# Performance work log

Measured on AMD Instinct MI355X. Metric: run time of the kernel, lower is better.

The kernel has to match this reference:

```python
import jax, jax.numpy as jnp
import numpy as np

B, C, R = 1024, 256, 7          # batch, channels, ROI feature map res
PATCH, DIL = 16, 2              # correlation patch size, dilation_patch
REP = 1024                      # representation_size
FLAT = PATCH * PATCH * R * R    # 12544 = fc1 input dim


def setup_inputs() -> dict:
    key = jax.random.key(0)
    k = jax.random.split(key, 8)
    return {
        "patch1": jax.random.normal(k[0], (B, C, R, R), dtype=jnp.float32),
        "patch2": jax.random.normal(k[1], (B, C, R, R), dtype=jnp.float32),
        "W1": jax.random.normal(k[2], (REP, FLAT), dtype=jnp.float32) * 0.01,
        "b1": jnp.zeros((REP,), dtype=jnp.float32),
        "W2": jax.random.normal(k[3], (REP, REP), dtype=jnp.float32) * 0.02,
        "b2": jnp.zeros((REP,), dtype=jnp.float32),
        "W3": jax.random.normal(k[4], (4, REP), dtype=jnp.float32) * 0.02,
        "b3": jnp.zeros((4,), dtype=jnp.float32),
    }


def _correlate(p1, p2):
    """SpatialCorrelationSampler(patch_size=16, dilation_patch=2), kernel=1, stride=1.
    out[b, pi, pj, i, j] = sum_c p1[b,c,i,j] * p2[b,c, i+(pi-8)*2, j+(pj-8)*2]
    (zero outside bounds). Returns [B, PATCH*PATCH, R, R]."""
    pad = (PATCH // 2) * DIL  # 16; displacements span [-16, 14]
    p2p = jnp.pad(p2, ((0, 0), (0, 0), (pad, pad), (pad, pad)))  # [B,C,39,39]
    outs = []
    for pi in range(PATCH):
        for pj in range(PATCH):
            # shifted window: row offset (pi-8)*2 + pad = 2*pi, same for cols
            win = p2p[:, :, DIL * pi:DIL * pi + R, DIL * pj:DIL * pj + R]
            outs.append(jnp.einsum('bchw,bchw->bhw', p1, win))
    return jnp.stack(outs, axis=1)  # [B, 256, 7, 7] -> matches torch flatten order


def reference(patch1, patch2, W1, b1, W2, b2, W3, b3):
    x = _correlate(patch1, patch2).reshape(patch1.shape[0], -1)  # [B, 12544]
    x = jax.nn.relu(x @ W1.T + b1)
    x = jax.nn.relu(x @ W2.T + b2)
    pred_boxes = x @ W3.T + b3  # [B, 4]
    return pred_boxes
```

## Files before the change

### kernel.cpp

```cpp
#include <hip/hip_runtime.h>

#define BATCH 1024
#define RR    49
#define SP    12544
#define KVALID 625
#define KPAD   640
#define REP_N  1024

typedef __attribute__((ext_vector_type(4))) float f32x4;
typedef __attribute__((ext_vector_type(8))) short s16x8;

__device__ __forceinline__ unsigned short f2bf_rne(float f) {
    unsigned int u = __float_as_uint(f);
    unsigned int r = u + 0x7FFFu + ((u >> 16) & 1u);
    return (unsigned short)(r >> 16);
}
__device__ __forceinline__ float bf2f(unsigned short h) {
    return __uint_as_float(((unsigned int)h) << 16);
}
__device__ __forceinline__ void split2(float v, unsigned short& h, unsigned short& l) {
    h = f2bf_rne(v);
    l = f2bf_rne(v - bf2f(h));
}
__device__ __forceinline__ unsigned int cvtpk_bf16(float a, float b) {
    unsigned int r;
    asm("v_cvt_pk_bf16_f32 %0, %1, %2" : "=v"(r) : "v"(a), "v"(b));
    return r;
}
__device__ __forceinline__ void cvt8(const float* v, s16x8& hv, s16x8& lv) {
    unsigned int* hp = (unsigned int*)&hv;
    unsigned int* lp = (unsigned int*)&lv;
    #pragma unroll
    for (int i = 0; i < 4; ++i) {
        float v0 = v[2 * i], v1 = v[2 * i + 1];
        unsigned int ph = cvtpk_bf16(v0, v1);
        float h0 = __uint_as_float(ph << 16);
        float h1 = __uint_as_float(ph & 0xFFFF0000u);
        unsigned int pl = cvtpk_bf16(v0 - h0, v1 - h1);
        hp[i] = ph; lp[i] = pl;
    }
}

__device__ __forceinline__ void dec25(int u, int& i, int& d) {
    int ii = (u >= 4) + (u >= 7) + (u >= 11) + (u >= 14) + (u >= 18) + (u >= 21);
    int cum = (7 * ii + 1) >> 1;
    i = ii;
    d = 2 * (u - cum) + (ii & 1);
}
__device__ __forceinline__ int enc25(int i, int d) {
    return ((7 * i + 1) >> 1) + ((d - (i & 1)) >> 1);
}

__device__ __forceinline__ int kflat_of(int a) {
    int ar = a / 25, ac = a % 25;
    int i, dy, j, dx;
    dec25(ar, i, dy);
    dec25(ac, j, dx);
    int pi = (dy + 16 - i) >> 1;
    int pj = (dx + 16 - j) >> 1;
    return (pi * 16 + pj) * 49 + i * 7 + j;
}

#define MM(d, a, b) d = __builtin_amdgcn_mfma_f32_16x16x32_bf16(a, b, d, 0, 0, 0)

__global__ __launch_bounds__(256) void corr_gram_kernel(
    const float* __restrict__ p1, const float* __restrict__ p2,
    unsigned short* __restrict__ xh, unsigned short* __restrict__ xl)
{
    __shared__ unsigned short SXh[KPAD];
    __shared__ unsigned short SXl[KPAD];

    const int b = blockIdx.x;
    const int t = threadIdx.x;
    const float* P1 = p1 + (size_t)b * SP;
    const float* P2 = p2 + (size_t)b * SP;

    const int wv   = t >> 6;
    const int lane = t & 63;
    const int wr = (wv >> 1) * 32;
    const int wc = (wv & 1) * 32;
    const int fr = lane & 15;
    const int fg = (lane >> 4) * 8;

    const int sa0 = wr + fr;
    const int sa1 = min(wr + 16 + fr, 48);
    const int sb0 = wc + fr;
    const int sb1 = min(wc + 16 + fr, 48);

    const float* pa0 = P1 + fg * 49 + sa0;
    const float* pa1 = P1 + fg * 49 + sa1;
    const float* pb0 = P2 + fg * 49 + sb0;
    const float* pb1 = P2 + fg * 49 + sb1;

    for (int i = t; i < KPAD; i += 256) { SXh[i] = 0; SXl[i] = 0; }

    f32x4 acc00 = {}, acc01 = {}, acc10 = {}, acc11 = {};

    #pragma unroll
    for (int cc = 0; cc < 4; ++cc) {
        #pragma unroll
        for (int ks = 0; ks < 2; ++ks) {
            const int co = (cc * 64 + ks * 32) * 49;
            float a0f[8], a1f[8], b0f[8], b1f[8];
            #pragma unroll
            for (int i = 0; i < 8; ++i) {
                a0f[i] = pa0[co + i * 49];
                a1f[i] = pa1[co + i * 49];
                b0f[i] = pb0[co + i * 49];
                b1f[i] = pb1[co + i * 49];
            }
            s16x8 ah0, al0, ah1, al1, bh0, bl0, bh1, bl1;
            cvt8(a0f, ah0, al0);
            cvt8(a1f, ah1, al1);
            cvt8(b0f, bh0, bl0);
            cvt8(b1f, bh1, bl1);

            MM(acc00, ah0, bh0); MM(acc00, ah0, bl0); MM(acc00, al0, bh0);
            MM(acc01, ah0, bh1); MM(acc01, ah0, bl1); MM(acc01, al0, bh1);
            MM(acc10, ah1, bh0); MM(acc10, ah1, bl0); MM(acc10, al1, bh0);
            MM(acc11, ah1, bh1); MM(acc11, ah1, bl1); MM(acc11, al1, bh1);
        }
    }

    const int arow = (lane >> 4) * 4;
    #pragma unroll
    for (int nf = 0; nf < 2; ++nf) {
        const int n = wc + nf * 16 + fr;
        #pragma unroll
        for (int mf = 0; mf < 2; ++mf) {
            const f32x4 a = (nf == 0) ? (mf == 0 ? acc00 : acc10)
                                      : (mf == 0 ? acc01 : acc11);
            #pragma unroll
            for (int r = 0; r < 4; ++r) {
                const int m = wr + mf * 16 + arow + r;
                if (m < RR && n < RR) {
                    const int i  = m / 7, jj = m - i * 7;
                    const int dy = n / 7, dx = n - dy * 7;
                    if ((((i + dy) | (jj + dx)) & 1) == 0) {
                        const int aidx = enc25(i, dy) * 25 + enc25(jj, dx);
                        unsigned short h, l;
                        split2(a[r], h, l);
                        SXh[aidx] = h; SXl[aidx] = l;
                    }
                }
            }
        }
    }
    __syncthreads();

    unsigned int* rh = (unsigned int*)(xh + (size_t)b * KPAD);
    unsigned int* rl = (unsigned int*)(xl + (size_t)b * KPAD);
    const unsigned int* sh = (const unsigned int*)SXh;
    const unsigned int* sl = (const unsigned int*)SXl;
    for (int i = t; i < KPAD / 2; i += 256) { rh[i] = sh[i]; rl[i] = sl[i]; }
}

__global__ __launch_bounds__(256) void prep_w1_kernel(
    const float* __restrict__ W1,
    unsigned short* __restrict__ wh, unsigned short* __restrict__ wl)
{
    int idx = blockIdx.x * 256 + threadIdx.x;
    int n = idx / KPAD, a = idx - n * KPAD;
    float v = 0.f;
    if (a < KVALID) v = W1[(size_t)n * SP + kflat_of(a)];
    unsigned short h, l;
    split2(v, h, l);
    wh[idx] = h; wl[idx] = l;
}

__global__ __launch_bounds__(256) void prep_w2_kernel(
    const float* __restrict__ W2,
    unsigned short* __restrict__ wh, unsigned short* __restrict__ wl)
{
    int idx = (blockIdx.x * 256 + threadIdx.x) * 4;
    float4 v = *(const float4*)&W2[idx];
    unsigned short h0, l0, h1, l1, h2, l2, h3, l3;
    split2(v.x, h0, l0); split2(v.y, h1, l1);
    split2(v.z, h2, l2); split2(v.w, h3, l3);
    ushort4 hv = make_ushort4(h0, h1, h2, h3);
    ushort4 lv = make_ushort4(l0, l1, l2, l3);
    *(ushort4*)&wh[idx] = hv;
    *(ushort4*)&wl[idx] = lv;
}

template<bool SPLIT_OUT>
__global__ __launch_bounds__(256) void gemm_mfma(
    const unsigned short* __restrict__ Xh, const unsigned short* __restrict__ Xl, int ldx,
    const unsigned short* __restrict__ Wh, const unsigned short* __restrict__ Wl, int ldw,
    const float* __restrict__ bias, int K,
    float* __restrict__ Yf, unsigned short* __restrict__ Yh, unsigned short* __restrict__ Yl,
    int ldy)
{
    __shared__ unsigned short As[2][64][72];
    __shared__ unsigned short Bs[2][64][72];

    const int t = threadIdx.x;
    const int m_base = blockIdx.y * 64;
    const int n_base = blockIdx.x * 64;

    const int trow = t >> 2;
    const int tc   = (t & 3) * 8;

    const unsigned short* xh_p = Xh + (size_t)(m_base + trow) * ldx + tc;
    const unsigned short* xl_p = Xl + (size_t)(m_base + trow) * ldx + tc;
    const unsigned short* wh_p = Wh + (size_t)(n_base + trow) * ldw + tc;
    const unsigned short* wl_p = Wl + (size_t)(n_base + trow) * ldw + tc;

    const int wv   = t >> 6;
    const int lane = t & 63;
    const int wr = (wv >> 1) * 32;
    const int wc = (wv & 1) * 32;
    const int fr = lane & 15;
    const int fg = (lane >> 4) * 8;

    f32x4 acc00 = {}, acc01 = {}, acc10 = {}, acc11 = {};

    for (int k0 = 0; k0 < K; k0 += 64) {
        s16x8 vxh0 = *(const s16x8*)(xh_p + k0);
        s16x8 vxh1 = *(const s16x8*)(xh_p + k0 + 32);
        s16x8 vxl0 = *(const s16x8*)(xl_p + k0);
        s16x8 vxl1 = *(const s16x8*)(xl_p + k0 + 32);
        s16x8 vwh0 = *(const s16x8*)(wh_p + k0);
        s16x8 vwh1 = *(const s16x8*)(wh_p + k0 + 32);
        s16x8 vwl0 = *(const s16x8*)(wl_p + k0);
        s16x8 vwl1 = *(const s16x8*)(wl_p + k0 + 32);
        __syncthreads();
        *(s16x8*)&As[0][trow][tc]      = vxh0;
        *(s16x8*)&As[0][trow][tc + 32] = vxh1;
        *(s16x8*)&As[1][trow][tc]      = vxl0;
        *(s16x8*)&As[1][trow][tc + 32] = vxl1;
        *(s16x8*)&Bs[0][trow][tc]      = vwh0;
        *(s16x8*)&Bs[0][trow][tc + 32] = vwh1;
        *(s16x8*)&Bs[1][trow][tc]      = vwl0;
        *(s16x8*)&Bs[1][trow][tc + 32] = vwl1;
        __syncthreads();

        #pragma unroll
        for (int ks = 0; ks < 2; ++ks) {
            const int ko = ks * 32 + fg;
            s16x8 ah0 = *(const s16x8*)&As[0][wr + fr][ko];
            s16x8 ah1 = *(const s16x8*)&As[0][wr + 16 + fr][ko];
            s16x8 al0 = *(const s16x8*)&As[1][wr + fr][ko];
            s16x8 al1 = *(const s16x8*)&As[1][wr + 16 + fr][ko];
            s16x8 bh0 = *(const s16x8*)&Bs[0][wc + fr][ko];
            s16x8 bh1 = *(const s16x8*)&Bs[0][wc + 16 + fr][ko];
            s16x8 bl0 = *(const s16x8*)&Bs[1][wc + fr][ko];
            s16x8 bl1 = *(const s16x8*)&Bs[1][wc + 16 + fr][ko];

            MM(acc00, ah0, bh0); MM(acc00, ah0, bl0); MM(acc00, al0, bh0);
            MM(acc01, ah0, bh1); MM(acc01, ah0, bl1); MM(acc01, al0, bh1);
            MM(acc10, ah1, bh0); MM(acc10, ah1, bl0); MM(acc10, al1, bh0);
            MM(acc11, ah1, bh1); MM(acc11, ah1, bl1); MM(acc11, al1, bh1);
        }
    }

    const int arow = (lane >> 4) * 4;
    #pragma unroll
    for (int nf = 0; nf < 2; ++nf) {
        const int col = n_base + wc + nf * 16 + fr;
        const float bv = bias[col];
        #pragma unroll
        for (int mf = 0; mf < 2; ++mf) {
            const f32x4 a = (nf == 0) ? (mf == 0 ? acc00 : acc10)
                                      : (mf == 0 ? acc01 : acc11);
            #pragma unroll
            for (int r = 0; r < 4; ++r) {
                const int row = m_base + wr + mf * 16 + arow + r;
                float v = fmaxf(a[r] + bv, 0.f);
                if (SPLIT_OUT) {
                    unsigned short h, l;
                    split2(v, h, l);
                    Yh[(size_t)row * ldy + col] = h;
                    Yl[(size_t)row * ldy + col] = l;
                } else {
                    Yf[(size_t)row * ldy + col] = v;
                }
            }
        }
    }
}

__global__ __launch_bounds__(256) void head_kernel(
    const float* __restrict__ h2, const float* __restrict__ W3,
    const float* __restrict__ b3, float* __restrict__ out)
{
    const int b = blockIdx.x;
    const int t = threadIdx.x;
    const float* row = h2 + (size_t)b * REP_N;

    float a0 = 0.f, a1 = 0.f, a2 = 0.f, a3 = 0.f;
    for (int k = t; k < REP_N; k += 256) {
        float x = row[k];
        a0 = fmaf(x, W3[k],             a0);
        a1 = fmaf(x, W3[REP_N + k],     a1);
        a2 = fmaf(x, W3[2 * REP_N + k], a2);
        a3 = fmaf(x, W3[3 * REP_N + k], a3);
    }
    #pragma unroll
    for (int off = 32; off > 0; off >>= 1) {
        a0 += __shfl_down(a0, off);
        a1 += __shfl_down(a1, off);
        a2 += __shfl_down(a2, off);
        a3 += __shfl_down(a3, off);
    }
    __shared__ float red[4][4];
    int wid = t >> 6, lane = t & 63;
    if (lane == 0) { red[wid][0] = a0; red[wid][1] = a1; red[wid][2] = a2; red[wid][3] = a3; }
    __syncthreads();
    if (t < 4) {
        out[b * 4 + t] = red[0][t] + red[1][t] + red[2][t] + red[3][t] + b3[t];
    }
}

extern "C" void kernel_launch(void* const* d_in, const int* in_sizes, int n_in,
                              void* d_out, int out_size, void* d_ws, size_t ws_size,
                              hipStream_t stream) {
    const float* p1 = (const float*)d_in[0];
    const float* p2 = (const float*)d_in[1];
    const float* W1 = (const float*)d_in[2];
    const float* b1 = (const float*)d_in[3];
    const float* W2 = (const float*)d_in[4];
    const float* b2 = (const float*)d_in[5];
    const float* W3 = (const float*)d_in[6];
    const float* b3 = (const float*)d_in[7];
    float* out = (float*)d_out;

    char* ws = (char*)d_ws;
    unsigned short* xh  = (unsigned short*)(ws + 0);
    unsigned short* xl  = (unsigned short*)(ws + 1310720);
    unsigned short* w1h = (unsigned short*)(ws + 2621440);
    unsigned short* w1l = (unsigned short*)(ws + 3932160);
    float*          h2  = (float*)(ws + 0);
    unsigned short* h1h = (unsigned short*)(ws + 5242880);
    unsigned short* h1l = (unsigned short*)(ws + 7340032);
    unsigned short* w2h = (unsigned short*)(ws + 9437184);
    unsigned short* w2l = (unsigned short*)(ws + 11534336);

    corr_gram_kernel<<<BATCH, 256, 0, stream>>>(p1, p2, xh, xl);
    prep_w1_kernel<<<(REP_N * KPAD) / 256, 256, 0, stream>>>(W1, w1h, w1l);
    prep_w2_kernel<<<(REP_N * REP_N) / (256 * 4), 256, 0, stream>>>(W2, w2h, w2l);

    gemm_mfma<true><<<dim3(16, 16), 256, 0, stream>>>(
        xh, xl, KPAD, w1h, w1l, KPAD, b1, KPAD,
        (float*)nullptr, h1h, h1l, REP_N);

    gemm_mfma<false><<<dim3(16, 16), 256, 0, stream>>>(
        h1h, h1l, REP_N, w2h, w2l, REP_N, b2, REP_N,
        h2, (unsigned short*)nullptr, (unsigned short*)nullptr, REP_N);

    head_kernel<<<BATCH, 256, 0, stream>>>(h2, W3, b3, out);
}
```

Before: 66.72 us.

## Split correlation Gram over channel halves with a separate reduction kernel

The per-batch correlation Gram kernel is split along the channel dimension into two blocks per batch. Each block writes fp32 partial sums to workspace, and a new reduce kernel sums them and does the bf16 hi/lo split. The goal is more blocks in flight and shorter per-block latency for the memory-bound correlation stage. The cost is an extra kernel launch plus an extra round trip of the partials through global memory.

Result: slower. 78.60 us (+17.8%).

```diff
diff --git a/kernel.cpp b/kernel.cpp
--- a/kernel.cpp
+++ b/kernel.cpp
@@ -6,6 +6,7 @@
 #define KVALID 625
 #define KPAD   640
 #define REP_N  1024
+#define KSPLIT 2
 
 typedef __attribute__((ext_vector_type(4))) float f32x4;
 typedef __attribute__((ext_vector_type(8))) short s16x8;
@@ -63,18 +64,18 @@
 
 #define MM(d, a, b) d = __builtin_amdgcn_mfma_f32_16x16x32_bf16(a, b, d, 0, 0, 0)
 
-__global__ __launch_bounds__(256) void corr_gram_kernel(
+__global__ __launch_bounds__(256, 8) void corr_gram_partial(
     const float* __restrict__ p1, const float* __restrict__ p2,
-    unsigned short* __restrict__ xh, unsigned short* __restrict__ xl)
-{
-    __shared__ unsigned short SXh[KPAD];
-    __shared__ unsigned short SXl[KPAD];
+    float* __restrict__ pg)
+{
+    __shared__ float SXf[KPAD];
 
     const int b = blockIdx.x;
+    const int q = blockIdx.y;
+    const float* P1 = p1 + (size_t)b * SP + q * (256 / KSPLIT) * RR;
+    const float* P2 = p2 + (size_t)b * SP + q * (256 / KSPLIT) * RR;
+
     const int t = threadIdx.x;
-    const float* P1 = p1 + (size_t)b * SP;
-    const float* P2 = p2 + (size_t)b * SP;
-
     const int wv   = t >> 6;
     const int lane = t & 63;
     const int wr = (wv >> 1) * 32;
@@ -87,39 +88,36 @@
     const int sb0 = wc + fr;
     const int sb1 = min(wc + 16 + fr, 48);
 
-    const float* pa0 = P1 + fg * 49 + sa0;
-    const float* pa1 = P1 + fg * 49 + sa1;
-    const float* pb0 = P2 + fg * 49 + sb0;
-    const float* pb1 = P2 + fg * 49 + sb1;
-
-    for (int i = t; i < KPAD; i += 256) { SXh[i] = 0; SXl[i] = 0; }
+    const float* pa0 = P1 + fg * RR + sa0;
+    const float* pa1 = P1 + fg * RR + sa1;
+    const float* pb0 = P2 + fg * RR + sb0;
+    const float* pb1 = P2 + fg * RR + sb1;
+
+    for (int i = t; i < KPAD; i += 256) SXf[i] = 0.f;
 
     f32x4 acc00 = {}, acc01 = {}, acc10 = {}, acc11 = {};
 
     #pragma unroll
-    for (int cc = 0; cc < 4; ++cc) {
+    for (int kk = 0; kk < (256 / KSPLIT) / 32; ++kk) {
+        const int co = kk * 32 * RR;
+        float a0f[8], a1f[8], b0f[8], b1f[8];
         #pragma unroll
-        for (int ks = 0; ks < 2; ++ks) {
-            const int co = (cc * 64 + ks * 32) * 49;
-            float a0f[8], a1f[8], b0f[8], b1f[8];
-            #pragma unroll
-            for (int i = 0; i < 8; ++i) {
-                a0f[i] = pa0[co + i * 49];
-                a1f[i] = pa1[co + i * 49];
-                b0f[i] = pb0[co + i * 49];
-                b1f[i] = pb1[co + i * 49];
-            }
-            s16x8 ah0, al0, ah1, al1, bh0, bl0, bh1, bl1;
-            cvt8(a0f, ah0, al0);
-            cvt8(a1f, ah1, al1);
-            cvt8(b0f, bh0, bl0);
-            cvt8(b1f, bh1, bl1);
-
-            MM(acc00, ah0, bh0); MM(acc00, ah0, bl0); MM(acc00, al0, bh0);
-            MM(acc01, ah0, bh1); MM(acc01, ah0, bl1); MM(acc01, al0, bh1);
-            MM(acc10, ah1, bh0); MM(acc10, ah1, bl0); MM(acc10, al1, bh0);
-            MM(acc11, ah1, bh1); MM(acc11, ah1, bl1); MM(acc11, al1, bh1);
+        for (int i = 0; i < 8; ++i) {
+            a0f[i] = pa0[co + i * RR];
+            a1f[i] = pa1[co + i * RR];
+            b0f[i] = pb0[co + i * RR];
+            b1f[i] = pb1[co + i * RR];
         }
+        s16x8 ah0, al0, ah1, al1, bh0, bl0, bh1, bl1;
+        cvt8(a0f, ah0, al0);
+        cvt8(a1f, ah1, al1);
+        cvt8(b0f, bh0, bl0);
+        cvt8(b1f, bh1, bl1);
+
+        MM(acc00, ah0, bh0); MM(acc00, ah0, bl0); MM(acc00, al0, bh0);
+        MM(acc01, ah0, bh1); MM(acc01, ah0, bl1); MM(acc01, al0, bh1);
+        MM(acc10, ah1, bh0); MM(acc10, ah1, bl0); MM(acc10, al1, bh0);
+        MM(acc11, ah1, bh1); MM(acc11, ah1, bl1); MM(acc11, al1, bh1);
     }
 
     const int arow = (lane >> 4) * 4;
@@ -138,9 +136,7 @@
                     const int dy = n / 7, dx = n - dy * 7;
                     if ((((i + dy) | (jj + dx)) & 1) == 0) {
                         const int aidx = enc25(i, dy) * 25 + enc25(jj, dx);
-                        unsigned short h, l;
-                        split2(a[r], h, l);
-                        SXh[aidx] = h; SXl[aidx] = l;
+                        SXf[aidx] = a[r];
                     }
                 }
             }
@@ -148,11 +144,23 @@
     }
     __syncthreads();
 
-    unsigned int* rh = (unsigned int*)(xh + (size_t)b * KPAD);
-    unsigned int* rl = (unsigned int*)(xl + (size_t)b * KPAD);
-    const unsigned int* sh = (const unsigned int*)SXh;
-    const unsigned int* sl = (const unsigned int*)SXl;
-    for (int i = t; i < KPAD / 2; i += 256) { rh[i] = sh[i]; rl[i] = sl[i]; }
+    float* dst = pg + ((size_t)b * KSPLIT + q) * KPAD;
+    for (int i = t; i < KPAD; i += 256) dst[i] = SXf[i];
+}
+
+__global__ __launch_bounds__(256) void reduce_x_kernel(
+    const float* __restrict__ pg,
+    unsigned short* __restrict__ xh, unsigned short* __restrict__ xl)
+{
+    int idx = blockIdx.x * 256 + threadIdx.x;
+    int b = idx / KPAD, a = idx - b * KPAD;
+    float s = 0.f;
+    #pragma unroll
+    for (int qq = 0; qq < KSPLIT; ++qq)
+        s += pg[((size_t)b * KSPLIT + qq) * KPAD + a];
+    unsigned short h, l;
+    split2(s, h, l);
+    xh[idx] = h; xl[idx] = l;
 }
 
 __global__ __launch_bounds__(256) void prep_w1_kernel(
@@ -335,10 +343,12 @@
     unsigned short* h1l = (unsigned short*)(ws + 7340032);
     unsigned short* w2h = (unsigned short*)(ws + 9437184);
     unsigned short* w2l = (unsigned short*)(ws + 11534336);
-
-    corr_gram_kernel<<<BATCH, 256, 0, stream>>>(p1, p2, xh, xl);
+    float*          pg  = (float*)(ws + 13631488);
+
+    corr_gram_partial<<<dim3(BATCH, KSPLIT), 256, 0, stream>>>(p1, p2, pg);
     prep_w1_kernel<<<(REP_N * KPAD) / 256, 256, 0, stream>>>(W1, w1h, w1l);
     prep_w2_kernel<<<(REP_N * REP_N) / (256 * 4), 256, 0, stream>>>(W2, w2h, w2l);
+    reduce_x_kernel<<<(BATCH * KPAD) / 256, 256, 0, stream>>>(pg, xh, xl);
 
     gemm_mfma<true><<<dim3(16, 16), 256, 0, stream>>>(
         xh, xl, KPAD, w1h, w1l, KPAD, b1, KPAD,
```

## Stage correlation inputs through padded LDS with register prefetch of next chunk

Applied to the files above, without the earlier changes.

The gram kernel used to read p1/p2 directly from global memory with strided scalar loads, one per MFMA operand element. It now loads each 64-channel chunk cooperatively with coalesced loads into registers and stores it into LDS padded to 53 floats per row to avoid bank conflicts. It prefetches the next chunk into registers while the MFMAs run on the current one. This adds about 27 KB of LDS, extra barriers and register pressure, and launch bounds now request 4 blocks per SM.

Result: slower. 70.23 us (+5.3%).

```diff
diff --git a/kernel.cpp b/kernel.cpp
--- a/kernel.cpp
+++ b/kernel.cpp
@@ -6,6 +6,7 @@
 #define KVALID 625
 #define KPAD   640
 #define REP_N  1024
+#define LP    53
 
 typedef __attribute__((ext_vector_type(4))) float f32x4;
 typedef __attribute__((ext_vector_type(8))) short s16x8;
@@ -63,10 +64,12 @@
 
 #define MM(d, a, b) d = __builtin_amdgcn_mfma_f32_16x16x32_bf16(a, b, d, 0, 0, 0)
 
-__global__ __launch_bounds__(256) void corr_gram_kernel(
+__global__ __launch_bounds__(256, 4) void corr_gram_kernel(
     const float* __restrict__ p1, const float* __restrict__ p2,
     unsigned short* __restrict__ xh, unsigned short* __restrict__ xl)
 {
+    __shared__ float T1[64 * LP];
+    __shared__ float T2[64 * LP];
     __shared__ unsigned short SXh[KPAD];
     __shared__ unsigned short SXl[KPAD];
 
@@ -86,28 +89,55 @@
     const int sa1 = min(wr + 16 + fr, 48);
     const int sb0 = wc + fr;
     const int sb1 = min(wc + 16 + fr, 48);
-
-    const float* pa0 = P1 + fg * 49 + sa0;
-    const float* pa1 = P1 + fg * 49 + sa1;
-    const float* pb0 = P2 + fg * 49 + sb0;
-    const float* pb1 = P2 + fg * 49 + sb1;
+    const int ra0 = fg * LP + sa0;
+    const int ra1 = fg * LP + sa1;
+    const int rb0 = fg * LP + sb0;
+    const int rb1 = fg * LP + sb1;
 
     for (int i = t; i < KPAD; i += 256) { SXh[i] = 0; SXl[i] = 0; }
 
+    float r1[13], r2[13];
+    #pragma unroll
+    for (int k = 0; k < 13; ++k) {
+        const int g = t + k * 256;
+        if (g < 3136) { r1[k] = P1[g]; r2[k] = P2[g]; }
+    }
+
     f32x4 acc00 = {}, acc01 = {}, acc10 = {}, acc11 = {};
 
     #pragma unroll
     for (int cc = 0; cc < 4; ++cc) {
+        __syncthreads();
+        #pragma unroll
+        for (int k = 0; k < 13; ++k) {
+            const int g = t + k * 256;
+            if (g < 3136) {
+                const int addr = g + 4 * (g / 49);
+                T1[addr] = r1[k];
+                T2[addr] = r2[k];
+            }
+        }
+        __syncthreads();
+
+        if (cc < 3) {
+            const int off = (cc + 1) * 3136;
+            #pragma unroll
+            for (int k = 0; k < 13; ++k) {
+                const int g = t + k * 256;
+                if (g < 3136) { r1[k] = P1[off + g]; r2[k] = P2[off + g]; }
+            }
+        }
+
         #pragma unroll
         for (int ks = 0; ks < 2; ++ks) {
-            const int co = (cc * 64 + ks * 32) * 49;
+            const int ko = ks * 32 * LP;
             float a0f[8], a1f[8], b0f[8], b1f[8];
             #pragma unroll
             for (int i = 0; i < 8; ++i) {
-                a0f[i] = pa0[co + i * 49];
-                a1f[i] = pa1[co + i * 49];
-                b0f[i] = pb0[co + i * 49];
-                b1f[i] = pb1[co + i * 49];
+                a0f[i] = T1[ra0 + ko + i * LP];
+                a1f[i] = T1[ra1 + ko + i * LP];
+                b0f[i] = T2[rb0 + ko + i * LP];
+                b1f[i] = T2[rb1 + ko + i * LP];
             }
             s16x8 ah0, al0, ah1, al1, bh0, bl0, bh1, bl1;
             cvt8(a0f, ah0, al0);
```

## Compute correlation Gram only within spatial parity classes via LDS staging

Applied to the files above, without the earlier changes.

The correlation kernel used to compute the full 49x49 Gram matrix per batch item with four MFMA tiles per wave and then discard entries with mismatched parity. Now each wave handles one of the four (row, column) parity classes, which needs only a single 16x16 tile, so MFMA work drops to a quarter. Inputs are loaded with coalesced float4 reads and staged through padded LDS tiles one 64-channel chunk at a time, with the next chunk prefetched into registers. The cost is extra LDS traffic and two barriers per chunk, plus a larger shared-memory footprint that may lower occupancy.

After: 66.42 us. Within noise of the previous version (-0.4%).

```diff
diff --git a/kernel.cpp b/kernel.cpp
--- a/kernel.cpp
+++ b/kernel.cpp
@@ -6,6 +6,7 @@
 #define KVALID 625
 #define KPAD   640
 #define REP_N  1024
+#define LP    53
 
 typedef __attribute__((ext_vector_type(4))) float f32x4;
 typedef __attribute__((ext_vector_type(8))) short s16x8;
@@ -63,10 +64,12 @@
 
 #define MM(d, a, b) d = __builtin_amdgcn_mfma_f32_16x16x32_bf16(a, b, d, 0, 0, 0)
 
-__global__ __launch_bounds__(256) void corr_gram_kernel(
+__global__ __launch_bounds__(256) void corr_parity_kernel(
     const float* __restrict__ p1, const float* __restrict__ p2,
     unsigned short* __restrict__ xh, unsigned short* __restrict__ xl)
 {
+    __shared__ float T1[64 * LP];
+    __shared__ float T2[64 * LP];
     __shared__ unsigned short SXh[KPAD];
     __shared__ unsigned short SXl[KPAD];
 
@@ -77,72 +80,91 @@
 
     const int wv   = t >> 6;
     const int lane = t & 63;
-    const int wr = (wv >> 1) * 32;
-    const int wc = (wv & 1) * 32;
-    const int fr = lane & 15;
-    const int fg = (lane >> 4) * 8;
-
-    const int sa0 = wr + fr;
-    const int sa1 = min(wr + 16 + fr, 48);
-    const int sb0 = wc + fr;
-    const int sb1 = min(wc + 16 + fr, 48);
-
-    const float* pa0 = P1 + fg * 49 + sa0;
-    const float* pa1 = P1 + fg * 49 + sa1;
-    const float* pb0 = P2 + fg * 49 + sb0;
-    const float* pb1 = P2 + fg * 49 + sb1;
+    const int fr   = lane & 15;
+    const int fg   = (lane >> 4) * 8;
+
+    const int ci = wv >> 1, cj = wv & 1;
+    const int nj = 4 - cj;
+    const int clsN = (4 - ci) * nj;
+    const int pr = (fr < clsN) ? fr : 0;
+    const int sPos = (2 * (pr / nj) + ci) * 7 + (2 * (pr % nj) + cj);
 
     for (int i = t; i < KPAD; i += 256) { SXh[i] = 0; SXl[i] = 0; }
 
-    f32x4 acc00 = {}, acc01 = {}, acc10 = {}, acc11 = {};
-
+    float4 f1[4], f2[4];
     #pragma unroll
+    for (int q = 0; q < 4; ++q) {
+        const int qi = t + q * 256;
+        if (qi < 784) {
+            f1[q] = ((const float4*)P1)[qi];
+            f2[q] = ((const float4*)P2)[qi];
+        }
+    }
+
+    f32x4 acc = {};
+
     for (int cc = 0; cc < 4; ++cc) {
+        __syncthreads();
+        #pragma unroll
+        for (int q = 0; q < 4; ++q) {
+            const int qi = t + q * 256;
+            if (qi < 784) {
+                const int gg = qi * 4;
+                const float v1[4] = {f1[q].x, f1[q].y, f1[q].z, f1[q].w};
+                const float v2[4] = {f2[q].x, f2[q].y, f2[q].z, f2[q].w};
+                #pragma unroll
+                for (int e = 0; e < 4; ++e) {
+                    const int ch = (gg + e) / 49;
+                    const int s  = (gg + e) - ch * 49;
+                    T1[ch * LP + s] = v1[e];
+                    T2[ch * LP + s] = v2[e];
+                }
+            }
+        }
+        __syncthreads();
+
+        if (cc < 3) {
+            const float4* G1 = (const float4*)(P1 + (cc + 1) * 3136);
+            const float4* G2 = (const float4*)(P2 + (cc + 1) * 3136);
+            #pragma unroll
+            for (int q = 0; q < 4; ++q) {
+                const int qi = t + q * 256;
+                if (qi < 784) { f1[q] = G1[qi]; f2[q] = G2[qi]; }
+            }
+        }
+
         #pragma unroll
         for (int ks = 0; ks < 2; ++ks) {
-            const int co = (cc * 64 + ks * 32) * 49;
-            float a0f[8], a1f[8], b0f[8], b1f[8];
+            const int kb = (ks * 32 + fg) * LP + sPos;
+            float av[8], bv[8];
             #pragma unroll
             for (int i = 0; i < 8; ++i) {
-                a0f[i] = pa0[co + i * 49];
-                a1f[i] = pa1[co + i * 49];
-                b0f[i] = pb0[co + i * 49];
-                b1f[i] = pb1[co + i * 49];
-            }
-            s16x8 ah0, al0, ah1, al1, bh0, bl0, bh1, bl1;
-            cvt8(a0f, ah0, al0);
-            cvt8(a1f, ah1, al1);
-            cvt8(b0f, bh0, bl0);
-            cvt8(b1f, bh1, bl1);
-
-            MM(acc00, ah0, bh0); MM(acc00, ah0, bl0); MM(acc00, al0, bh0);
-            MM(acc01, ah0, bh1); MM(acc01, ah0, bl1); MM(acc01, al0, bh1);
-            MM(acc10, ah1, bh0); MM(acc10, ah1, bl0); MM(acc10, al1, bh0);
-            MM(acc11, ah1, bh1); MM(acc11, ah1, bl1); MM(acc11, al1, bh1);
+                av[i] = T1[kb + i * LP];
+                bv[i] = T2[kb + i * LP];
+            }
+            s16x8 ah, al, bh, bl;
+            cvt8(av, ah, al);
+            cvt8(bv, bh, bl);
+            MM(acc, ah, bh);
+            MM(acc, ah, bl);
+            MM(acc, al, bh);
         }
     }
 
     const int arow = (lane >> 4) * 4;
-    #pragma unroll
-    for (int nf = 0; nf < 2; ++nf) {
-        const int n = wc + nf * 16 + fr;
-        #pragma unroll
-        for (int mf = 0; mf < 2; ++mf) {
-            const f32x4 a = (nf == 0) ? (mf == 0 ? acc00 : acc10)
-                                      : (mf == 0 ? acc01 : acc11);
-            #pragma unroll
-            for (int r = 0; r < 4; ++r) {
-                const int m = wr + mf * 16 + arow + r;
-                if (m < RR && n < RR) {
-                    const int i  = m / 7, jj = m - i * 7;
-                    const int dy = n / 7, dx = n - dy * 7;
-                    if ((((i + dy) | (jj + dx)) & 1) == 0) {
-                        const int aidx = enc25(i, dy) * 25 + enc25(jj, dx);
-                        unsigned short h, l;
-                        split2(a[r], h, l);
-                        SXh[aidx] = h; SXl[aidx] = l;
-                    }
-                }
+    if (fr < clsN) {
+        const int dy = 2 * (fr / nj) + ci;
+        const int dx = 2 * (fr % nj) + cj;
+        #pragma unroll
+        for (int r = 0; r < 4; ++r) {
+            const int rowp = arow + r;
+            if (rowp < clsN) {
+                const int i1 = 2 * (rowp / nj) + ci;
+                const int j1 = 2 * (rowp % nj) + cj;
+                const int aidx = enc25(i1, dy) * 25 + enc25(j1, dx);
+                unsigned short h, l;
+                split2(acc[r], h, l);
+                SXh[aidx] = h; SXl[aidx] = l;
             }
         }
     }
@@ -177,10 +199,8 @@
     unsigned short h0, l0, h1, l1, h2, l2, h3, l3;
     split2(v.x, h0, l0); split2(v.y, h1, l1);
     split2(v.z, h2, l2); split2(v.w, h3, l3);
-    ushort4 hv = make_ushort4(h0, h1, h2, h3);
-    ushort4 lv = make_ushort4(l0, l1, l2, l3);
-    *(ushort4*)&wh[idx] = hv;
-    *(ushort4*)&wl[idx] = lv;
+    *(ushort4*)&wh[idx] = make_ushort4(h0, h1, h2, h3);
+    *(ushort4*)&wl[idx] = make_ushort4(l0, l1, l2, l3);
 }
 
 template<bool SPLIT_OUT>
@@ -336,7 +356,7 @@
     unsigned short* w2h = (unsigned short*)(ws + 9437184);
     unsigned short* w2l = (unsigned short*)(ws + 11534336);
 
-    corr_gram_kernel<<<BATCH, 256, 0, stream>>>(p1, p2, xh, xl);
+    corr_parity_kernel<<<BATCH, 256, 0, stream>>>(p1, p2, xh, xl);
     prep_w1_kernel<<<(REP_N * KPAD) / 256, 256, 0, stream>>>(W1, w1h, w1l);
     prep_w2_kernel<<<(REP_N * REP_N) / (256 * 4), 256, 0, stream>>>(W2, w2h, w2l);
 
```
